# Performance work log

Hardware: AMD Instinct MI355X
Metric: run time of the kernel (lower is better)

The kernel has to match this reference:

```python
import jax, jax.numpy as jnp
import numpy as np

N, D, E = 50000, 128, 800000


def setup_inputs() -> dict:
    key = jax.random.key(0)
    ks = jax.random.split(key, 12)
    x0 = jax.random.normal(ks[0], (N, D), dtype=jnp.float32)
    x1 = jax.random.normal(ks[1], (N, D), dtype=jnp.float32)
    edge_index = jax.random.randint(ks[2], (2, E), 0, N, dtype=jnp.int64)
    s = 0.05
    W1 = jax.random.normal(ks[3], (D, D), dtype=jnp.float32) * s
    b1 = jax.random.normal(ks[4], (D,), dtype=jnp.float32) * s
    W2 = jax.random.normal(ks[5], (D, D), dtype=jnp.float32) * s
    b2 = jax.random.normal(ks[6], (D,), dtype=jnp.float32) * s
    a1_w = jax.random.normal(ks[7], (D,), dtype=jnp.float32) * s
    a1_b = jax.random.normal(ks[8], (), dtype=jnp.float32) * s
    a2_w = jax.random.normal(ks[9], (D,), dtype=jnp.float32) * s
    a2_b = jax.random.normal(ks[10], (), dtype=jnp.float32) * s
    return {"x0": x0, "x1": x1, "edge_index": edge_index,
            "W1": W1, "b1": b1, "W2": W2, "b2": b2,
            "a1_w": a1_w, "a1_b": a1_b, "a2_w": a2_w, "a2_b": a2_b}


def reference(x0, x1, edge_index, W1, b1, W2, b2, a1_w, a1_b, a2_w, a2_b):
    # LeakyReLU(0.2) applied to both projections
    lrelu = lambda v: jnp.where(v >= 0, v, 0.2 * v)
    x0_i = lrelu(x0 @ W1.T + b1)          # [N, D]
    x0_j = lrelu(x0 @ W2.T + b2)          # [N, D]
    a1 = x0_i @ a1_w + a1_b               # [N]
    a2 = x0_j @ a2_w + a2_b               # [N]
    src, dst = edge_index[0], edge_index[1]
    # sigmoid(a_1 + a_2.T) evaluated only at the sparse edge indices
    att = jax.nn.sigmoid(a1[src] + a2[dst])            # [E]
    msg = att[:, None] * x0_j[dst]                     # [E, D]
    out = jax.ops.segment_sum(msg, src, num_segments=x0.shape[0])  # sparse.mm
    return out + x0
```

## Files before the change

kernel.cpp:

```cpp
#include <hip/hip_runtime.h>
#include <hip/hip_bf16.h>

typedef unsigned int u32;
typedef unsigned short u16;

#define DIM 128
#define LWS 136
#define CHUNK 2048

typedef __bf16 bfrag __attribute__((ext_vector_type(8)));
typedef float  facc  __attribute__((ext_vector_type(4)));

__device__ __forceinline__ float2 bfpair(u32 u) {
    union { u32 i; float f; } lo, hi;
    lo.i = (u & 0xFFFFu) << 16;
    hi.i = u & 0xFFFF0000u;
    return make_float2(lo.f, hi.f);
}
__device__ __forceinline__ float bf1(u16 h) {
    union { u32 i; float f; } a; a.i = ((u32)h) << 16; return a.f;
}
__device__ __forceinline__ u16 f2bf(float f) {
    __hip_bfloat16 h = __float2bfloat16(f);
    return *reinterpret_cast<u16*>(&h);
}
__device__ __forceinline__ u32 packbf(float x, float y) {
    return (u32)f2bf(x) | ((u32)f2bf(y) << 16);
}
__device__ __forceinline__ float ldfr(const void* p, int i, bool isbf) {
    return isbf ? bf1(((const u16*)p)[i]) : ((const float*)p)[i];
}

__global__ __launch_bounds__(64) void sniff_kernel(const u32* __restrict__ x0w,
                                                   const int* __restrict__ eiw,
                                                   int* __restrict__ flags) {
    int l = threadIdx.x;
    u32 w = x0w[l];
    u32 ef = (w >> 7) & 0xFF;
    bool inr = (ef >= 99 && ef <= 141);
    unsigned long long m1 = __ballot(inr);
    bool zodd = (eiw[2 * l + 1] == 0);
    unsigned long long m2 = __ballot(zodd);
    if (l == 0) {
        flags[0] = (__popcll(m1) >= 48) ? 1 : 0;
        flags[1] = (__popcll(m2) >= 32) ? 1 : 0;
    }
}

__global__ __launch_bounds__(256) void cvt_count_kernel(
    const float* __restrict__ x0, const float* __restrict__ W1,
    const float* __restrict__ W2, u16* __restrict__ x0c, u16* __restrict__ Wc,
    const int* __restrict__ ei, u32* __restrict__ keys0, int* __restrict__ cnt,
    const int* __restrict__ flags, int nx, int ne, int nblk, int ncvt)
{
    __shared__ int h[256];
    const int b = blockIdx.x, t = threadIdx.x;

    if (b < ncvt) {
        if (flags[0] != 0) return;
        int i = b * 256 + t;
        if (i >= nx + 4096) return;
        const float* src; u16* dst; int c;
        if (i < nx) { src = x0; dst = x0c; c = i; }
        else {
            int j = i - nx;
            src = (j < 2048) ? W1 : W2;
            dst = Wc + ((j < 2048) ? 0 : 16384);
            c = j & 2047;
        }
        float4 f0 = ((const float4*)src)[c * 2];
        float4 f1 = ((const float4*)src)[c * 2 + 1];
        uint4 u = make_uint4(packbf(f0.x, f0.y), packbf(f0.z, f0.w),
                             packbf(f1.x, f1.y), packbf(f1.z, f1.w));
        ((uint4*)dst)[c] = u;
        return;
    }

    const int hb = b - ncvt;
    if (hb >= nblk) return;
    h[t] = 0;
    __syncthreads();
    const bool i64 = flags[1] != 0;
    const int base = hb * CHUNK;
    #pragma unroll
    for (int r = 0; r < CHUNK / 256; ++r) {
        int i = base + r * 256 + t;
        if (i < ne) {
            int src = i64 ? ei[2 * i] : ei[i];
            int dst = i64 ? ei[2 * (ne + i)] : ei[ne + i];
            u32 key = ((u32)src << 16) | (u32)dst;
            keys0[i] = key;
            atomicAdd(&h[key >> 24], 1);
        }
    }
    __syncthreads();
    cnt[t * nblk + hb] = h[t];
}

__global__ __launch_bounds__(256) void proj_scan_kernel(
    const void* __restrict__ x0v, const u16* __restrict__ x0c,
    const void* __restrict__ W1v, const void* __restrict__ b1v,
    const void* __restrict__ W2v, const void* __restrict__ b2v,
    const void* __restrict__ a1wv, const void* __restrict__ a1bv,
    const void* __restrict__ a2wv, const void* __restrict__ a2bv,
    const u16* __restrict__ Wc,
    u16* __restrict__ xj, float* __restrict__ a1, float* __restrict__ a2,
    const int* __restrict__ cnt, int* __restrict__ off, int* __restrict__ tot,
    const int* __restrict__ flags, int n, int nchunk, int bpg, int nblk)
{
    __shared__ u16 lw[128 * LWS];
    __shared__ int v[512];
    const int b = blockIdx.x, t = threadIdx.x;

    if (b < 256) {
        const int d = b;
        int c0 = (t < nblk) ? cnt[d * nblk + t] : 0;
        int c1 = (t + 256 < nblk) ? cnt[d * nblk + t + 256] : 0;
        v[t] = c0; v[t + 256] = c1;
        __syncthreads();
        for (int s = 1; s < 512; s <<= 1) {
            int a0 = v[t],       b0 = (t >= s) ? v[t - s] : 0;
            int a1v = v[t + 256], b1v = (t + 256 >= s) ? v[t + 256 - s] : 0;
            __syncthreads();
            v[t] = a0 + b0; v[t + 256] = a1v + b1v;
            __syncthreads();
        }
        if (t < nblk)       off[d * nblk + t]       = v[t] - c0;
        if (t + 256 < nblk) off[d * nblk + t + 256] = v[t + 256] - c1;
        if (t == 0) tot[d] = v[511];
        return;
    }

    const bool isbf = flags[0] != 0;
    const int pid = b - 256;
    const int grp = pid / bpg;
    const int cb  = pid % bpg;

    const u16* x0s  = isbf ? (const u16*)x0v : x0c;
    const u16* Ws   = isbf ? (const u16*)(grp ? W2v : W1v) : (Wc + grp * 16384);
    const void* bv  = grp ? b2v  : b1v;
    const void* awv = grp ? a2wv : a1wv;
    const void* abv = grp ? a2bv : a1bv;
    float* aout     = grp ? a2   : a1;

    for (int j = t; j < 2048; j += 256) {
        int r = j >> 4, c = j & 15;
        *(uint4*)(lw + (size_t)r * LWS + c * 8) =
            *(const uint4*)(Ws + (size_t)r * DIM + c * 8);
    }
    __syncthreads();

    const int wid = t >> 6, l = t & 63;
    const int chunk = cb * 4 + wid;
    if (chunk >= nchunk) return;
    const int r0 = chunk * 32;
    const int lr = l & 15;
    const int q  = l >> 4;

    bfrag a[2][4];
    #pragma unroll
    for (int rt = 0; rt < 2; ++rt) {
        int row = min(r0 + rt * 16 + lr, n - 1);
        #pragma unroll
        for (int k = 0; k < 4; ++k) {
            const uint4* p = (const uint4*)(x0s + (size_t)row * DIM + k * 32 + q * 8);
            a[rt][k] = __builtin_bit_cast(bfrag, *p);
        }
    }

    facc acc[2][8];
    #pragma unroll
    for (int rt = 0; rt < 2; ++rt)
        #pragma unroll
        for (int ct = 0; ct < 8; ++ct)
            acc[rt][ct] = (facc){0.f, 0.f, 0.f, 0.f};

    #pragma unroll
    for (int ct = 0; ct < 8; ++ct) {
        bfrag bb[4];
        const u16* lrow = lw + (size_t)(ct * 16 + lr) * LWS;
        #pragma unroll
        for (int k = 0; k < 4; ++k)
            bb[k] = *(const bfrag*)(lrow + k * 32 + q * 8);
        #pragma unroll
        for (int rt = 0; rt < 2; ++rt)
            #pragma unroll
            for (int k = 0; k < 4; ++k)
                acc[rt][ct] = __builtin_amdgcn_mfma_f32_16x16x32_bf16(
                    a[rt][k], bb[k], acc[rt][ct], 0, 0, 0);
    }

    float s[2][4] = {{0.f,0.f,0.f,0.f},{0.f,0.f,0.f,0.f}};
    #pragma unroll
    for (int ct = 0; ct < 8; ++ct) {
        float bc  = ldfr(bv,  ct * 16 + lr, isbf);
        float awc = ldfr(awv, ct * 16 + lr, isbf);
        #pragma unroll
        for (int rt = 0; rt < 2; ++rt)
            #pragma unroll
            for (int reg = 0; reg < 4; ++reg) {
                float vv = acc[rt][ct][reg] + bc;
                vv = vv >= 0.f ? vv : 0.2f * vv;
                int row = r0 + rt * 16 + q * 4 + reg;
                if (grp && row < n)
                    xj[(size_t)row * DIM + ct * 16 + lr] = f2bf(vv);
                s[rt][reg] = fmaf(vv, awc, s[rt][reg]);
            }
    }
    #pragma unroll
    for (int o = 1; o < 16; o <<= 1)
        #pragma unroll
        for (int rt = 0; rt < 2; ++rt)
            #pragma unroll
            for (int reg = 0; reg < 4; ++reg)
                s[rt][reg] += __shfl_xor(s[rt][reg], o);
    if (lr == 0) {
        float ab = ldfr(abv, 0, isbf);
        #pragma unroll
        for (int rt = 0; rt < 2; ++rt)
            #pragma unroll
            for (int reg = 0; reg < 4; ++reg) {
                int row = r0 + rt * 16 + q * 4 + reg;
                if (row < n) aout[row] = s[rt][reg] + ab;
            }
    }
}

__global__ __launch_bounds__(256) void reorderH_kernel(
    const u32* __restrict__ kin, u32* __restrict__ kout,
    const int* __restrict__ off, const int* __restrict__ tot,
    int ne, int nblk)
{
    __shared__ int boff[256];
    __shared__ int sv[256];
    const int b = blockIdx.x, t = threadIdx.x;
    int c = tot[t];
    sv[t] = c;
    __syncthreads();
    for (int s = 1; s < 256; s <<= 1) {
        int a = sv[t], add = (t >= s) ? sv[t - s] : 0;
        __syncthreads();
        sv[t] = a + add;
        __syncthreads();
    }
    boff[t] = (sv[t] - c) + off[t * nblk + b];
    sv[t] = 0;
    __syncthreads();
    const int base = b * CHUNK;
    #pragma unroll
    for (int r = 0; r < CHUNK / 256; ++r) {
        int i = base + r * 256 + t;
        if (i < ne) {
            u32 key = kin[i];
            int d = key >> 24;
            int rk = atomicAdd(&sv[d], 1);
            kout[boff[d] + rk] = key;
        }
    }
}

__global__ __launch_bounds__(256) void bucket_kernel(
    const u32* __restrict__ keys1, const int* __restrict__ tot,
    const float* __restrict__ a1, const float* __restrict__ a2,
    int* __restrict__ ptr, u32* __restrict__ sorted, int n)
{
    __shared__ int cnt[256];
    __shared__ int sc[256];
    __shared__ int cur[256];
    __shared__ int bas[256];
    const int b = blockIdx.x, t = threadIdx.x;

    int c0 = tot[t];
    sc[t] = c0;
    __syncthreads();
    for (int s = 1; s < 256; s <<= 1) {
        int a = sc[t], add = (t >= s) ? sc[t - s] : 0;
        __syncthreads();
        sc[t] = a + add;
        __syncthreads();
    }
    bas[t] = sc[t] - c0;
    cnt[t] = 0;
    __syncthreads();
    const int base = bas[b];
    const int size = tot[b];

    for (int i = t; i < size; i += 256)
        atomicAdd(&cnt[(keys1[base + i] >> 16) & 0xFF], 1);
    __syncthreads();
    int c = cnt[t];
    sc[t] = c;
    __syncthreads();
    for (int s = 1; s < 256; s <<= 1) {
        int a = sc[t], add = (t >= s) ? sc[t - s] : 0;
        __syncthreads();
        sc[t] = a + add;
        __syncthreads();
    }
    int ex = sc[t] - c;
    cur[t] = ex;
    int sg = (b << 8) + t;
    if (sg <= n) ptr[sg] = base + ex;
    __syncthreads();
    for (int i = t; i < size; i += 256) {
        u32 key = keys1[base + i];
        int j   = (key >> 16) & 0xFF;
        int rk  = atomicAdd(&cur[j], 1);
        int src = (int)(key >> 16);
        int dst = (int)(key & 0xFFFFu);
        float av  = a1[src] + a2[dst];
        float att = 1.0f / (1.0f + __expf(-av));
        u32 a16 = (u32)lrintf(att * 65535.0f);
        sorted[base + rk] = (a16 << 16) | (u32)dst;
    }
}

#define ATTDEC(r) ((float)((r) >> 16) * (1.0f / 65535.0f))

__global__ __launch_bounds__(256) void gather_kernel(
    const int* __restrict__ ptr, const u32* __restrict__ sorted,
    const u32* __restrict__ xjw, const void* __restrict__ x0v,
    void* __restrict__ outv, const int* __restrict__ flags, int n)
{
    const bool bf16 = flags[0] != 0;
    int s = blockIdx.x * 4 + (threadIdx.x >> 6);
    int l = threadIdx.x & 63;
    if (s >= n) return;

    float2 acc0, acc1;
    if (bf16) acc0 = bfpair(((const u32*)x0v)[(size_t)s * 64 + l]);
    else      acc0 = ((const float2*)x0v)[(size_t)s * 64 + l];
    acc1 = make_float2(0.f, 0.f);

    int k = ptr[s], end = ptr[s + 1];

    while (k + 16 <= end) {
        u32 r[16];
        #pragma unroll
        for (int j = 0; j < 16; ++j) r[j] = sorted[k + j];
        u32 w[16];
        #pragma unroll
        for (int j = 0; j < 16; ++j) w[j] = xjw[(size_t)(r[j] & 0xFFFFu) * 64 + l];
        #pragma unroll
        for (int j = 0; j < 16; ++j) {
            float att = ATTDEC(r[j]);
            float2 xv = bfpair(w[j]);
            if (j & 1) { acc1.x = fmaf(att, xv.x, acc1.x);
                         acc1.y = fmaf(att, xv.y, acc1.y); }
            else       { acc0.x = fmaf(att, xv.x, acc0.x);
                         acc0.y = fmaf(att, xv.y, acc0.y); }
        }
        k += 16;
    }
    if (k + 8 <= end) {
        u32 r[8];
        #pragma unroll
        for (int j = 0; j < 8; ++j) r[j] = sorted[k + j];
        u32 w[8];
        #pragma unroll
        for (int j = 0; j < 8; ++j) w[j] = xjw[(size_t)(r[j] & 0xFFFFu) * 64 + l];
        #pragma unroll
        for (int j = 0; j < 8; ++j) {
            float att = ATTDEC(r[j]);
            float2 xv = bfpair(w[j]);
            if (j & 1) { acc1.x = fmaf(att, xv.x, acc1.x);
                         acc1.y = fmaf(att, xv.y, acc1.y); }
            else       { acc0.x = fmaf(att, xv.x, acc0.x);
                         acc0.y = fmaf(att, xv.y, acc0.y); }
        }
        k += 8;
    }
    if (k + 4 <= end) {
        u32 r[4];
        #pragma unroll
        for (int j = 0; j < 4; ++j) r[j] = sorted[k + j];
        u32 w[4];
        #pragma unroll
        for (int j = 0; j < 4; ++j) w[j] = xjw[(size_t)(r[j] & 0xFFFFu) * 64 + l];
        #pragma unroll
        for (int j = 0; j < 4; ++j) {
            float att = ATTDEC(r[j]);
            float2 xv = bfpair(w[j]);
            if (j & 1) { acc1.x = fmaf(att, xv.x, acc1.x);
                         acc1.y = fmaf(att, xv.y, acc1.y); }
            else       { acc0.x = fmaf(att, xv.x, acc0.x);
                         acc0.y = fmaf(att, xv.y, acc0.y); }
        }
        k += 4;
    }
    for (; k < end; ++k) {
        u32 cur = sorted[k];
        float att = ATTDEC(cur);
        float2 xv = bfpair(xjw[(size_t)(cur & 0xFFFFu) * 64 + l]);
        acc0.x = fmaf(att, xv.x, acc0.x);
        acc0.y = fmaf(att, xv.y, acc0.y);
    }
    acc0.x += acc1.x;
    acc0.y += acc1.y;

    if (bf16) ((u32*)outv)[(size_t)s * 64 + l] = packbf(acc0.x, acc0.y);
    else      ((float2*)outv)[(size_t)s * 64 + l] = acc0;
}

extern "C" void kernel_launch(void* const* d_in, const int* in_sizes, int n_in,
                              void* d_out, int out_size, void* d_ws, size_t ws_size,
                              hipStream_t stream)
{
    const void* x0  = d_in[0];
    const int*  ei  = (const int*)d_in[2];
    const void* W1  = d_in[3];
    const void* b1  = d_in[4];
    const void* W2  = d_in[5];
    const void* b2  = d_in[6];
    const void* a1w = d_in[7];
    const void* a1b = d_in[8];
    const void* a2w = d_in[9];
    const void* a2b = d_in[10];

    const int n = in_sizes[0] / DIM;
    const int e = in_sizes[2] / 2;
    const int nblk = (e + CHUNK - 1) / CHUNK;

    char* ws = (char*)d_ws;
    int* flags = (int*)ws;
    size_t off = 1024;
    u16* xj = (u16*)(ws + off);
    off += (size_t)n * DIM * sizeof(u16);   off = (off + 255) & ~(size_t)255;
    u16* x0c = (u16*)(ws + off);
    off += (size_t)n * DIM * sizeof(u16);   off = (off + 255) & ~(size_t)255;
    u16* Wc = (u16*)(ws + off);
    off += (size_t)2 * 16384 * sizeof(u16); off = (off + 255) & ~(size_t)255;
    float* a1 = (float*)(ws + off);
    off += (size_t)n * sizeof(float);       off = (off + 255) & ~(size_t)255;
    float* a2 = (float*)(ws + off);
    off += (size_t)n * sizeof(float);       off = (off + 255) & ~(size_t)255;
    u32* keys0 = (u32*)(ws + off);
    off += (size_t)e * sizeof(u32);         off = (off + 255) & ~(size_t)255;
    u32* keys1 = (u32*)(ws + off);
    off += (size_t)e * sizeof(u32);         off = (off + 255) & ~(size_t)255;
    int* cntH = (int*)(ws + off);
    off += (size_t)256 * nblk * sizeof(int); off = (off + 255) & ~(size_t)255;
    int* offH = (int*)(ws + off);
    off += (size_t)256 * nblk * sizeof(int); off = (off + 255) & ~(size_t)255;
    int* totH = (int*)(ws + off);  off += 1024;
    int* ptr = (int*)(ws + off);
    off += (size_t)(n + 1) * sizeof(int);   off = (off + 255) & ~(size_t)255;
    u32* sorted = (u32*)(ws + off);

    sniff_kernel<<<1, 64, 0, stream>>>((const u32*)x0, ei, flags);

    const int nx = n * DIM / 8;
    const int ncvt = (nx + 4096 + 255) / 256;
    cvt_count_kernel<<<ncvt + nblk, 256, 0, stream>>>((const float*)x0,
        (const float*)W1, (const float*)W2, x0c, Wc, ei, keys0, cntH,
        flags, nx, e, nblk, ncvt);

    const int nchunk = (n + 31) / 32;
    const int bpg = (nchunk + 3) / 4;
    proj_scan_kernel<<<256 + 2 * bpg, 256, 0, stream>>>(x0, x0c, W1, b1, W2, b2,
        a1w, a1b, a2w, a2b, Wc, xj, a1, a2, cntH, offH, totH, flags,
        n, nchunk, bpg, nblk);

    reorderH_kernel<<<nblk, 256, 0, stream>>>(keys0, keys1, offH, totH, e, nblk);

    const int nbucket = (n >> 8) + 1;
    bucket_kernel<<<nbucket, 256, 0, stream>>>(keys1, totH, a1, a2,
                                               ptr, sorted, n);

    int gblocks = (n + 3) / 4;
    gather_kernel<<<gblocks, 256, 0, stream>>>(ptr, sorted, (const u32*)xj,
                                               x0, d_out, flags, n);
}
```

Baseline: 191.8 us.

## Gather four edges per wavefront with 16-byte row loads and shuffle reduction

```diff
diff --git a/kernel.cpp b/kernel.cpp
--- a/kernel.cpp
+++ b/kernel.cpp
@@ -326,80 +326,57 @@
     int s = blockIdx.x * 4 + (threadIdx.x >> 6);
     int l = threadIdx.x & 63;
     if (s >= n) return;
-
-    float2 acc0, acc1;
-    if (bf16) acc0 = bfpair(((const u32*)x0v)[(size_t)s * 64 + l]);
-    else      acc0 = ((const float2*)x0v)[(size_t)s * 64 + l];
-    acc1 = make_float2(0.f, 0.f);
-
-    int k = ptr[s], end = ptr[s + 1];
-
-    while (k + 16 <= end) {
-        u32 r[16];
-        #pragma unroll
-        for (int j = 0; j < 16; ++j) r[j] = sorted[k + j];
-        u32 w[16];
-        #pragma unroll
-        for (int j = 0; j < 16; ++j) w[j] = xjw[(size_t)(r[j] & 0xFFFFu) * 64 + l];
-        #pragma unroll
-        for (int j = 0; j < 16; ++j) {
-            float att = ATTDEC(r[j]);
-            float2 xv = bfpair(w[j]);
-            if (j & 1) { acc1.x = fmaf(att, xv.x, acc1.x);
-                         acc1.y = fmaf(att, xv.y, acc1.y); }
-            else       { acc0.x = fmaf(att, xv.x, acc0.x);
-                         acc0.y = fmaf(att, xv.y, acc0.y); }
-        }
-        k += 16;
-    }
-    if (k + 8 <= end) {
-        u32 r[8];
-        #pragma unroll
-        for (int j = 0; j < 8; ++j) r[j] = sorted[k + j];
-        u32 w[8];
-        #pragma unroll
-        for (int j = 0; j < 8; ++j) w[j] = xjw[(size_t)(r[j] & 0xFFFFu) * 64 + l];
-        #pragma unroll
-        for (int j = 0; j < 8; ++j) {
-            float att = ATTDEC(r[j]);
-            float2 xv = bfpair(w[j]);
-            if (j & 1) { acc1.x = fmaf(att, xv.x, acc1.x);
-                         acc1.y = fmaf(att, xv.y, acc1.y); }
-            else       { acc0.x = fmaf(att, xv.x, acc0.x);
-                         acc0.y = fmaf(att, xv.y, acc0.y); }
-        }
-        k += 8;
-    }
-    if (k + 4 <= end) {
+    const int g = l >> 4;
+    const int c = l & 15;
+
+    float2 m0 = make_float2(0.f, 0.f), m1 = make_float2(0.f, 0.f);
+    float2 m2 = make_float2(0.f, 0.f), m3 = make_float2(0.f, 0.f);
+
+    int k = ptr[s];
+    const int end = ptr[s + 1];
+
+    while (k < end) {
         u32 r[4];
         #pragma unroll
-        for (int j = 0; j < 4; ++j) r[j] = sorted[k + j];
-        u32 w[4];
-        #pragma unroll
-        for (int j = 0; j < 4; ++j) w[j] = xjw[(size_t)(r[j] & 0xFFFFu) * 64 + l];
+        for (int j = 0; j < 4; ++j) {
+            int idx = k + 4 * j + g;
+            r[j] = (idx < end) ? sorted[idx] : 0u;
+        }
+        uint4 w[4];
+        #pragma unroll
+        for (int j = 0; j < 4; ++j)
+            w[j] = ((const uint4*)(xjw + (size_t)(r[j] & 0xFFFFu) * 64))[c];
         #pragma unroll
         for (int j = 0; j < 4; ++j) {
             float att = ATTDEC(r[j]);
-            float2 xv = bfpair(w[j]);
-            if (j & 1) { acc1.x = fmaf(att, xv.x, acc1.x);
-                         acc1.y = fmaf(att, xv.y, acc1.y); }
-            else       { acc0.x = fmaf(att, xv.x, acc0.x);
-                         acc0.y = fmaf(att, xv.y, acc0.y); }
-        }
-        k += 4;
-    }
-    for (; k < end; ++k) {
-        u32 cur = sorted[k];
-        float att = ATTDEC(cur);
-        float2 xv = bfpair(xjw[(size_t)(cur & 0xFFFFu) * 64 + l]);
-        acc0.x = fmaf(att, xv.x, acc0.x);
-        acc0.y = fmaf(att, xv.y, acc0.y);
-    }
-    acc0.x += acc1.x;
-    acc0.y += acc1.y;
-
-    if (bf16) ((u32*)outv)[(size_t)s * 64 + l] = packbf(acc0.x, acc0.y);
-    else      ((float2*)outv)[(size_t)s * 64 + l] = acc0;
+            float2 v0 = bfpair(w[j].x), v1 = bfpair(w[j].y);
+            float2 v2 = bfpair(w[j].z), v3 = bfpair(w[j].w);
+            m0.x = fmaf(att, v0.x, m0.x); m0.y = fmaf(att, v0.y, m0.y);
+            m1.x = fmaf(att, v1.x, m1.x); m1.y = fmaf(att, v1.y, m1.y);
+            m2.x = fmaf(att, v2.x, m2.x); m2.y = fmaf(att, v2.y, m2.y);
+            m3.x = fmaf(att, v3.x, m3.x); m3.y = fmaf(att, v3.y, m3.y);
+        }
+        k += 16;
+    }
+
+    #pragma unroll
+    for (int o = 16; o < 64; o <<= 1) {
+        m0.x += __shfl_xor(m0.x, o); m0.y += __shfl_xor(m0.y, o);
+        m1.x += __shfl_xor(m1.x, o); m1.y += __shfl_xor(m1.y, o);
+        m2.x += __shfl_xor(m2.x, o); m2.y += __shfl_xor(m2.y, o);
+        m3.x += __shfl_xor(m3.x, o); m3.y += __shfl_xor(m3.y, o);
+    }
+
+    float2 m = (g == 0) ? m0 : (g == 1) ? m1 : (g == 2) ? m2 : m3;
+    const int slot = c * 4 + g;
+    if (bf16) {
+        float2 x0p = bfpair(((const u32*)x0v)[(size_t)s * 64 + slot]);
+        ((u32*)outv)[(size_t)s * 64 + slot] = packbf(m.x + x0p.x, m.y + x0p.y);
+    } else {
+        float2 x0p = ((const float2*)x0v)[(size_t)s * 64 + slot];
+        float2 o; o.x = m.x + x0p.x; o.y = m.y + x0p.y;
+        ((float2*)outv)[(size_t)s * 64 + slot] = o;
+    }
 }
 
 extern "C" void kernel_launch(void* const* d_in, const int* in_sizes, int n_in,
```

After: 191.5 us. No clear change (-0.2%).
